# Kernel tuning notes

Hardware: AMD Instinct MI355X
Metric: run time of the kernel (lower is better)

The kernel has to match this reference:

```python
import jax, jax.numpy as jnp
import numpy as np

N_NODES = 40000
N_EDGES = 640000
BATCH = 2
IN_DIM = 3
HID = 128
OUT_DIM = 3


def setup_inputs() -> dict:
    key = jax.random.key(0)
    ks = jax.random.split(key, 16)
    p = jax.random.normal(ks[0], (BATCH, N_NODES, IN_DIM), dtype=jnp.float32)
    edge_rows = jax.random.randint(ks[1], (N_EDGES,), 0, N_NODES, dtype=jnp.int32)
    edge_cols = jax.random.randint(ks[2], (N_EDGES,), 0, N_NODES, dtype=jnp.int32)
    # normalize_sparse_matrix: divide each nonzero (value 1.0) by the row's nonzero count
    deg = jax.ops.segment_sum(jnp.ones((N_EDGES,), jnp.float32), edge_rows, num_segments=N_NODES)
    adj_vals = 1.0 / deg[edge_rows]  # every used row has deg >= 1
    s = 0.05
    # initial Linear(3 -> 128)
    W_init = jax.random.normal(ks[3], (IN_DIM, HID), jnp.float32) * s
    b_init = jnp.zeros((HID,), jnp.float32)
    # 4 GraphConvs inside the two blocks (all 128->128), each has filter + self_filter
    Wf_blocks = jax.random.normal(ks[4], (4, HID, HID), jnp.float32) * s
    bf_blocks = jnp.zeros((4, HID), jnp.float32)
    Ws_blocks = jax.random.normal(ks[5], (4, HID, HID), jnp.float32) * s
    bs_blocks = jnp.zeros((4, HID), jnp.float32)
    # final GraphConvLayer (128 -> 3)
    Wf_out = jax.random.normal(ks[6], (HID, OUT_DIM), jnp.float32) * s
    bf_out = jnp.zeros((OUT_DIM,), jnp.float32)
    Ws_out = jax.random.normal(ks[7], (HID, OUT_DIM), jnp.float32) * s
    bs_out = jnp.zeros((OUT_DIM,), jnp.float32)
    return dict(p=p, adj_vals=adj_vals, edge_rows=edge_rows, edge_cols=edge_cols,
                W_init=W_init, b_init=b_init,
                Wf_blocks=Wf_blocks, bf_blocks=bf_blocks,
                Ws_blocks=Ws_blocks, bs_blocks=bs_blocks,
                Wf_out=Wf_out, bf_out=bf_out, Ws_out=Ws_out, bs_out=bs_out)


def reference(p, adj_vals, edge_rows, edge_cols,
              W_init, b_init,
              Wf_blocks, bf_blocks, Ws_blocks, bs_blocks,
              Wf_out, bf_out, Ws_out, bs_out):
    n = p.shape[1]

    def spmm(xb):  # xb: [N, d] -> A @ xb via edge-list scatter-add
        return jax.ops.segment_sum(adj_vals[:, None] * xb[edge_cols], edge_rows, num_segments=n)

    spmm_b = jax.vmap(spmm)  # [B, N, d]

    def gconv(x, Wf, bf, Ws, bs):
        # sparse path: self_filter(x) + filter(spmm(adj, x))
        return (x @ Ws + bs) + (spmm_b(x) @ Wf + bf)

    x = p @ W_init + b_init  # [B, N, HID]
    for blk in range(2):  # two GraphConvBlocks, residual, no shortcut (dims equal)
        net = gconv(jax.nn.relu(x), Wf_blocks[2 * blk], bf_blocks[2 * blk],
                    Ws_blocks[2 * blk], bs_blocks[2 * blk])
        dx = gconv(jax.nn.relu(net), Wf_blocks[2 * blk + 1], bf_blocks[2 * blk + 1],
                   Ws_blocks[2 * blk + 1], bs_blocks[2 * blk + 1])
        x = x + dx
    # final GraphConvLayer 128 -> 3
    out = gconv(jax.nn.relu(x), Wf_out, bf_out, Ws_out, bs_out)
    return out
```

## Files before the change

### kernel.cpp

```cpp
#include <hip/hip_runtime.h>


typedef unsigned short u16;
typedef unsigned int   u32;
typedef __bf16 bf8_t __attribute__((ext_vector_type(8)));
typedef float  f4_t  __attribute__((ext_vector_type(4)));

#define N_NODES 40000
#define N_EDGES 640000
#define BN      80000

__device__ __forceinline__ float bf2f(u16 u) {
  union { u32 i; float f; } v; v.i = ((u32)u) << 16; return v.f;
}
__device__ __forceinline__ u16 f2bf(float f) {
  union { float f; u32 i; } v; v.f = f;
  u32 i = v.i;
  return (u16)((i + 0x7FFFu + ((i >> 16) & 1u)) >> 16);
}
__device__ __forceinline__ float asf(u32 i) {
  union { u32 u; float f; } v; v.u = i; return v.f;
}
__device__ __forceinline__ u32 pack2(float a, float b) {
  return (u32)f2bf(a) | ((u32)f2bf(b) << 16);
}

__global__ void fill_kernel(float* __restrict__ out, int n, float v) {
  int i = blockIdx.x * 256 + threadIdx.x;
  if (i < n) out[i] = v;
}

__global__ void hist_kernel(const int* __restrict__ rows, int* __restrict__ cnt) {
  int e = blockIdx.x * 256 + threadIdx.x;
  if (e < N_EDGES) atomicAdd(&cnt[rows[e]], 1);
}

__global__ void scan1_kernel(const int* __restrict__ cnt, int* __restrict__ row_ptr,
                             int* __restrict__ blocksum) {
  __shared__ int sm[256];
  int t = threadIdx.x;
  int row = blockIdx.x * 256 + t;
  int v = (row < N_NODES) ? cnt[row] : 0;
  sm[t] = v; __syncthreads();
  for (int off = 1; off < 256; off <<= 1) {
    int u = (t >= off) ? sm[t - off] : 0;
    __syncthreads();
    sm[t] += u;
    __syncthreads();
  }
  if (row < N_NODES) row_ptr[row] = sm[t] - v;
  if (t == 255) blocksum[blockIdx.x] = sm[255];
}

__global__ void scan2_kernel(int* __restrict__ blocksum, int* __restrict__ row_ptr, int nblk) {
  __shared__ int sm[256];
  int t = threadIdx.x;
  int v = (t < nblk) ? blocksum[t] : 0;
  sm[t] = v; __syncthreads();
  for (int off = 1; off < 256; off <<= 1) {
    int u = (t >= off) ? sm[t - off] : 0;
    __syncthreads();
    sm[t] += u;
    __syncthreads();
  }
  if (t < nblk) blocksum[t] = sm[t] - v;
  if (t == 255) row_ptr[N_NODES] = sm[255];
}

__global__ void scan3_kernel(int* __restrict__ row_ptr, const int* __restrict__ blocksum,
                             int* __restrict__ cnt) {
  int row = blockIdx.x * 256 + threadIdx.x;
  if (row < N_NODES) {
    int rp = row_ptr[row] + blocksum[blockIdx.x];
    row_ptr[row] = rp;
    cnt[row] = rp;
  }
}

__global__ void scatter_kernel(const int* __restrict__ rows, const int* __restrict__ cols,
                               int* __restrict__ cur, int* __restrict__ cols_s) {
  int e = blockIdx.x * 256 + threadIdx.x;
  if (e < N_EDGES) {
    int r = rows[e];
    int pos = atomicAdd(&cur[r], 1);
    cols_s[pos] = cols[e];
  }
}

__global__ void wprep_kernel(const float* __restrict__ Wf_b, const float* __restrict__ Ws_b,
                             const float* __restrict__ bf_b, const float* __restrict__ bs_b,
                             u16* __restrict__ WtCat, float* __restrict__ biasCat) {
  int idx = blockIdx.x * 256 + threadIdx.x;
  int g = idx >> 15, rem = idx & 32767;
  int h = rem >> 8, k = rem & 255;
  float v = (k < 128) ? Ws_b[(g * 128 + k) * 128 + h]
                      : Wf_b[(g * 128 + (k - 128)) * 128 + h];
  WtCat[idx] = f2bf(v);
  if (k == 0) biasCat[g * 128 + h] = bs_b[g * 128 + h] + bf_b[g * 128 + h];
}

__global__ void init_kernel(const float* __restrict__ p, const float* __restrict__ W,
                            const float* __restrict__ bias, u16* __restrict__ xb,
                            u16* __restrict__ rA) {
  int idx = blockIdx.x * 256 + threadIdx.x;
  int row = idx >> 6;
  int h = (idx & 63) * 2;
  float p0 = p[row * 3], p1 = p[row * 3 + 1], p2 = p[row * 3 + 2];
  float s0 = p0 * W[h]     + p1 * W[128 + h]     + p2 * W[256 + h]     + bias[h];
  float s1 = p0 * W[h + 1] + p1 * W[128 + h + 1] + p2 * W[256 + h + 1] + bias[h + 1];
  size_t o = (size_t)row * 64 + (h >> 1);
  ((u32*)xb)[o] = pack2(s0, s1);
  ((u32*)rA)[o] = pack2(s0 > 0.f ? s0 : 0.f, s1 > 0.f ? s1 : 0.f);
}

__global__ void spmm_kernel(const int* __restrict__ row_ptr, const int* __restrict__ cols_s,
                            const u16* __restrict__ xin, u16* __restrict__ yout) {
  int row = blockIdx.x * 4 + (threadIdx.x >> 6);
  int l = threadIdx.x & 63;
  int b = l >> 5, seg = l & 31;
  int s = row_ptr[row], e = row_ptr[row + 1];
  const u32* X = (const u32*)xin + (size_t)b * 2560000 + seg * 2;
  float a0 = 0.f, a1 = 0.f, a2 = 0.f, a3 = 0.f;
  int i = s;
  for (; i + 1 < e; i += 2) {
    int c0 = cols_s[i], c1 = cols_s[i + 1];
    uint2 u0 = *reinterpret_cast<const uint2*>(X + (size_t)c0 * 64);
    uint2 u1 = *reinterpret_cast<const uint2*>(X + (size_t)c1 * 64);
    a0 += asf(u0.x << 16); a1 += asf(u0.x & 0xffff0000u);
    a2 += asf(u0.y << 16); a3 += asf(u0.y & 0xffff0000u);
    a0 += asf(u1.x << 16); a1 += asf(u1.x & 0xffff0000u);
    a2 += asf(u1.y << 16); a3 += asf(u1.y & 0xffff0000u);
  }
  if (i < e) {
    int c = cols_s[i];
    uint2 u = *reinterpret_cast<const uint2*>(X + (size_t)c * 64);
    a0 += asf(u.x << 16); a1 += asf(u.x & 0xffff0000u);
    a2 += asf(u.y << 16); a3 += asf(u.y & 0xffff0000u);
  }
  float scale = (e > s) ? 1.f / (float)(e - s) : 0.f;
  uint2 o;
  o.x = pack2(a0 * scale, a1 * scale);
  o.y = pack2(a2 * scale, a3 * scale);
  *reinterpret_cast<uint2*>((u32*)yout + (size_t)b * 2560000 + (size_t)row * 64 + seg * 2) = o;
}

template <int MODE>
__global__ __launch_bounds__(256, 2) void gemm_kernel(
    const u16* __restrict__ rin, const u16* __restrict__ yin,
    const u16* __restrict__ WtCat, const float* __restrict__ biasCat, int g,
    u16* __restrict__ rout, u16* __restrict__ xresid) {
  __shared__ __align__(16) u16 ldsA[128 * 72];
  __shared__ __align__(16) u16 ldsW[128 * 72];
  int tid = threadIdx.x;
  int m0 = blockIdx.x * 128;
  int li = tid & 15, q = (tid >> 4) & 3, wv = tid >> 6;
  int wmo = (wv >> 1) * 64, wno = (wv & 1) * 64;

  f4_t acc[4][4];
#pragma unroll
  for (int i = 0; i < 4; ++i)
#pragma unroll
    for (int j = 0; j < 4; ++j) acc[i][j] = (f4_t){0.f, 0.f, 0.f, 0.f};

  const u16* Wsrc = WtCat + (size_t)g * 32768;

  for (int kb = 0; kb < 256; kb += 64) {
    __syncthreads();
    const u16* srcA = (kb < 128) ? (rin + kb) : (yin + (kb - 128));
#pragma unroll
    for (int p2 = 0; p2 < 4; ++p2) {
      int idx = p2 * 256 + tid;
      int row = idx >> 3, seg = idx & 7;
      uint4 va = *reinterpret_cast<const uint4*>(srcA + (size_t)(m0 + row) * 128 + seg * 8);
      *reinterpret_cast<uint4*>(&ldsA[row * 72 + seg * 8]) = va;
      uint4 vw = *reinterpret_cast<const uint4*>(Wsrc + (size_t)row * 256 + kb + seg * 8);
      *reinterpret_cast<uint4*>(&ldsW[row * 72 + seg * 8]) = vw;
    }
    __syncthreads();
#pragma unroll
    for (int kk = 0; kk < 64; kk += 32) {
      bf8_t af[4], wf[4];
#pragma unroll
      for (int t = 0; t < 4; ++t)
        af[t] = __builtin_bit_cast(bf8_t,
            *reinterpret_cast<const uint4*>(&ldsA[(wmo + t * 16 + li) * 72 + kk + q * 8]));
#pragma unroll
      for (int t = 0; t < 4; ++t)
        wf[t] = __builtin_bit_cast(bf8_t,
            *reinterpret_cast<const uint4*>(&ldsW[(wno + t * 16 + li) * 72 + kk + q * 8]));
#pragma unroll
      for (int i = 0; i < 4; ++i)
#pragma unroll
        for (int j = 0; j < 4; ++j)
          acc[i][j] = __builtin_amdgcn_mfma_f32_16x16x32_bf16(af[i], wf[j], acc[i][j], 0, 0, 0);
    }
  }

  float bias[4];
#pragma unroll
  for (int j = 0; j < 4; ++j) bias[j] = biasCat[g * 128 + wno + j * 16 + li];

#pragma unroll
  for (int i = 0; i < 4; ++i)
#pragma unroll
    for (int j = 0; j < 4; ++j)
#pragma unroll
      for (int r2 = 0; r2 < 4; ++r2) {
        int m = m0 + wmo + i * 16 + q * 4 + r2;
        int col = wno + j * 16 + li;
        float c = acc[i][j][r2] + bias[j];
        size_t id = (size_t)m * 128 + col;
        if (MODE == 0) {
          rout[id] = f2bf(c > 0.f ? c : 0.f);
        } else {
          float xn = bf2f(xresid[id]) + c;
          xresid[id] = f2bf(xn);
          rout[id] = f2bf(xn > 0.f ? xn : 0.f);
        }
      }
}

__global__ void final_kernel(const u16* __restrict__ rA, const u16* __restrict__ y,
                             const float* __restrict__ Wso, const float* __restrict__ Wfo,
                             const float* __restrict__ bso, const float* __restrict__ bfo,
                             float* __restrict__ out) {
  int row = blockIdx.x * 4 + (threadIdx.x >> 6);
  int l = threadIdx.x & 63;
  u32 ra = ((const u32*)rA)[(size_t)row * 64 + l];
  u32 yv = ((const u32*)y)[(size_t)row * 64 + l];
  float r0 = asf(ra << 16), r1 = asf(ra & 0xffff0000u);
  float y0 = asf(yv << 16), y1 = asf(yv & 0xffff0000u);
  int ch = l * 2;
  float p0 = r0 * Wso[ch * 3 + 0] + y0 * Wfo[ch * 3 + 0] + r1 * Wso[ch * 3 + 3] + y1 * Wfo[ch * 3 + 3];
  float p1 = r0 * Wso[ch * 3 + 1] + y0 * Wfo[ch * 3 + 1] + r1 * Wso[ch * 3 + 4] + y1 * Wfo[ch * 3 + 4];
  float p2 = r0 * Wso[ch * 3 + 2] + y0 * Wfo[ch * 3 + 2] + r1 * Wso[ch * 3 + 5] + y1 * Wfo[ch * 3 + 5];
#pragma unroll
  for (int off = 32; off >= 1; off >>= 1) {
    p0 += __shfl_down(p0, off);
    p1 += __shfl_down(p1, off);
    p2 += __shfl_down(p2, off);
  }
  if (l == 0) {
    out[row * 3 + 0] = p0 + bso[0] + bfo[0];
    out[row * 3 + 1] = p1 + bso[1] + bfo[1];
    out[row * 3 + 2] = p2 + bso[2] + bfo[2];
  }
}

extern "C" void kernel_launch(void* const* d_in, const int* in_sizes, int n_in,
                              void* d_out, int out_size, void* d_ws, size_t ws_size,
                              hipStream_t stream) {
  float* out = (float*)d_out;
  int fill_grid = (out_size + 255) / 256;

  const int exp_sizes[14] = {240000, 640000, 640000, 640000, 384, 128,
                             65536, 512, 65536, 512, 384, 3, 384, 3};
  bool sizes_ok = (n_in == 14);
  if (sizes_ok) for (int i = 0; i < 14; ++i) if (in_sizes[i] != exp_sizes[i]) sizes_ok = false;
  if (!sizes_ok) {
    fill_kernel<<<fill_grid, 256, 0, stream>>>(out, out_size, 1.0f);
    return;
  }

  const size_t NEED = (size_t)4 * BN * 128 * 2 + (size_t)N_EDGES * 4 + 160016 + 160000 + 1024 + 262144 + 2048;
  if (ws_size < NEED) {
    fill_kernel<<<fill_grid, 256, 0, stream>>>(out, out_size, 0.0f);
    return;
  }

  const float* p      = (const float*)d_in[0];
  const int*   erows  = (const int*)d_in[2];
  const int*   ecols  = (const int*)d_in[3];
  const float* W_init = (const float*)d_in[4];
  const float* b_init = (const float*)d_in[5];
  const float* Wf_b   = (const float*)d_in[6];
  const float* bf_b   = (const float*)d_in[7];
  const float* Ws_b   = (const float*)d_in[8];
  const float* bs_b   = (const float*)d_in[9];
  const float* Wf_o   = (const float*)d_in[10];
  const float* bf_o   = (const float*)d_in[11];
  const float* Ws_o   = (const float*)d_in[12];
  const float* bs_o   = (const float*)d_in[13];

  char* w = (char*)d_ws;
  u16*   rA       = (u16*)w;   w += (size_t)BN * 128 * 2;
  u16*   rB       = (u16*)w;   w += (size_t)BN * 128 * 2;
  u16*   y        = (u16*)w;   w += (size_t)BN * 128 * 2;
  u16*   xb       = (u16*)w;   w += (size_t)BN * 128 * 2;
  int*   cols_s   = (int*)w;   w += (size_t)N_EDGES * 4;
  int*   row_ptr  = (int*)w;   w += 160016;
  int*   cnt      = (int*)w;   w += 160000;
  int*   blocksum = (int*)w;   w += 1024;
  u16*   WtCat    = (u16*)w;   w += 4 * 128 * 256 * 2;
  float* biasCat  = (float*)w; w += 4 * 128 * 4;

  const int NBLK = (N_NODES + 255) / 256;

  hipMemsetAsync(cnt, 0, N_NODES * 4, stream);
  hist_kernel<<<2500, 256, 0, stream>>>(erows, cnt);
  scan1_kernel<<<NBLK, 256, 0, stream>>>(cnt, row_ptr, blocksum);
  scan2_kernel<<<1, 256, 0, stream>>>(blocksum, row_ptr, NBLK);
  scan3_kernel<<<NBLK, 256, 0, stream>>>(row_ptr, blocksum, cnt);
  scatter_kernel<<<2500, 256, 0, stream>>>(erows, ecols, cnt, cols_s);
  wprep_kernel<<<512, 256, 0, stream>>>(Wf_b, Ws_b, bf_b, bs_b, WtCat, biasCat);
  init_kernel<<<20000, 256, 0, stream>>>(p, W_init, b_init, xb, rA);

  for (int blk = 0; blk < 2; ++blk) {
    spmm_kernel<<<10000, 256, 0, stream>>>(row_ptr, cols_s, rA, y);
    gemm_kernel<0><<<625, 256, 0, stream>>>(rA, y, WtCat, biasCat, 2 * blk, rB, nullptr);
    spmm_kernel<<<10000, 256, 0, stream>>>(row_ptr, cols_s, rB, y);
    gemm_kernel<1><<<625, 256, 0, stream>>>(rB, y, WtCat, biasCat, 2 * blk + 1, rA, xb);
  }
  spmm_kernel<<<10000, 256, 0, stream>>>(row_ptr, cols_s, rA, y);
  final_kernel<<<20000, 256, 0, stream>>>(rA, y, Ws_o, Wf_o, bs_o, bf_o, out);
}
```

Before: 510.0 us.

## Reassociate final layer to project before SpMM, widen SpMM loads, prefetch GEMM tiles

The final GraphConv now projects the 128-wide activations down to 3 channels first and only then aggregates over neighbours, using A(xW) = (Ax)W. This replaces a full 128-wide SpMM with a 3-wide one. The block SpMM now splits the batch across thread blocks and has each lane load 16-byte rows, with four lane groups handling different edges and combining through cross-lane shuffles. The GEMM adds register prefetch of the next K tile so global loads overlap the MFMA work. The reassociation changes rounding slightly, since the projection is taken from bf16 activations before aggregation.

```diff
diff --git a/kernel.cpp b/kernel.cpp
--- a/kernel.cpp
+++ b/kernel.cpp
@@ -113,35 +113,51 @@
   ((u32*)rA)[o] = pack2(s0 > 0.f ? s0 : 0.f, s1 > 0.f ? s1 : 0.f);
 }
 
+#define ACC8(u)                                                           \
+  a0 += asf((u).x << 16); a1 += asf((u).x & 0xffff0000u);                 \
+  a2 += asf((u).y << 16); a3 += asf((u).y & 0xffff0000u);                 \
+  a4 += asf((u).z << 16); a5 += asf((u).z & 0xffff0000u);                 \
+  a6 += asf((u).w << 16); a7 += asf((u).w & 0xffff0000u);
+
 __global__ void spmm_kernel(const int* __restrict__ row_ptr, const int* __restrict__ cols_s,
                             const u16* __restrict__ xin, u16* __restrict__ yout) {
-  int row = blockIdx.x * 4 + (threadIdx.x >> 6);
+  int b = blockIdx.x & 1;
+  int row = (blockIdx.x >> 1) * 4 + (threadIdx.x >> 6);
   int l = threadIdx.x & 63;
-  int b = l >> 5, seg = l & 31;
+  int g = l >> 4, sl = l & 15;
   int s = row_ptr[row], e = row_ptr[row + 1];
-  const u32* X = (const u32*)xin + (size_t)b * 2560000 + seg * 2;
-  float a0 = 0.f, a1 = 0.f, a2 = 0.f, a3 = 0.f;
+  const uint4* X = (const uint4*)xin + (size_t)b * 640000 + sl;
+  float a0 = 0.f, a1 = 0.f, a2 = 0.f, a3 = 0.f, a4 = 0.f, a5 = 0.f, a6 = 0.f, a7 = 0.f;
   int i = s;
-  for (; i + 1 < e; i += 2) {
-    int c0 = cols_s[i], c1 = cols_s[i + 1];
-    uint2 u0 = *reinterpret_cast<const uint2*>(X + (size_t)c0 * 64);
-    uint2 u1 = *reinterpret_cast<const uint2*>(X + (size_t)c1 * 64);
-    a0 += asf(u0.x << 16); a1 += asf(u0.x & 0xffff0000u);
-    a2 += asf(u0.y << 16); a3 += asf(u0.y & 0xffff0000u);
-    a0 += asf(u1.x << 16); a1 += asf(u1.x & 0xffff0000u);
-    a2 += asf(u1.y << 16); a3 += asf(u1.y & 0xffff0000u);
-  }
-  if (i < e) {
-    int c = cols_s[i];
-    uint2 u = *reinterpret_cast<const uint2*>(X + (size_t)c * 64);
-    a0 += asf(u.x << 16); a1 += asf(u.x & 0xffff0000u);
-    a2 += asf(u.y << 16); a3 += asf(u.y & 0xffff0000u);
-  }
-  float scale = (e > s) ? 1.f / (float)(e - s) : 0.f;
-  uint2 o;
-  o.x = pack2(a0 * scale, a1 * scale);
-  o.y = pack2(a2 * scale, a3 * scale);
-  *reinterpret_cast<uint2*>((u32*)yout + (size_t)b * 2560000 + (size_t)row * 64 + seg * 2) = o;
+  for (; i + 7 < e; i += 8) {
+    int c0 = cols_s[i + g], c1 = cols_s[i + 4 + g];
+    uint4 u0 = X[(size_t)c0 * 16];
+    uint4 u1 = X[(size_t)c1 * 16];
+    ACC8(u0); ACC8(u1);
+  }
+  for (; i + 3 < e; i += 4) {
+    int c = cols_s[i + g];
+    uint4 u = X[(size_t)c * 16];
+    ACC8(u);
+  }
+  if (i + g < e) {
+    int c = cols_s[i + g];
+    uint4 u = X[(size_t)c * 16];
+    ACC8(u);
+  }
+  a0 += __shfl_xor(a0, 16); a1 += __shfl_xor(a1, 16); a2 += __shfl_xor(a2, 16); a3 += __shfl_xor(a3, 16);
+  a4 += __shfl_xor(a4, 16); a5 += __shfl_xor(a5, 16); a6 += __shfl_xor(a6, 16); a7 += __shfl_xor(a7, 16);
+  a0 += __shfl_xor(a0, 32); a1 += __shfl_xor(a1, 32); a2 += __shfl_xor(a2, 32); a3 += __shfl_xor(a3, 32);
+  a4 += __shfl_xor(a4, 32); a5 += __shfl_xor(a5, 32); a6 += __shfl_xor(a6, 32); a7 += __shfl_xor(a7, 32);
+  if (g == 0) {
+    float sc = (e > s) ? 1.f / (float)(e - s) : 0.f;
+    uint4 o;
+    o.x = pack2(a0 * sc, a1 * sc);
+    o.y = pack2(a2 * sc, a3 * sc);
+    o.z = pack2(a4 * sc, a5 * sc);
+    o.w = pack2(a6 * sc, a7 * sc);
+    *((uint4*)yout + (size_t)b * 640000 + (size_t)row * 16 + sl) = o;
+  }
 }
 
 template <int MODE>
@@ -164,19 +180,33 @@
 
   const u16* Wsrc = WtCat + (size_t)g * 32768;
 
+  uint4 pa[4], pw[4];
+#pragma unroll
+  for (int p2 = 0; p2 < 4; ++p2) {
+    int idx = p2 * 256 + tid, row = idx >> 3, seg = idx & 7;
+    pa[p2] = *reinterpret_cast<const uint4*>(rin + (size_t)(m0 + row) * 128 + seg * 8);
+    pw[p2] = *reinterpret_cast<const uint4*>(Wsrc + (size_t)row * 256 + seg * 8);
+  }
+
   for (int kb = 0; kb < 256; kb += 64) {
     __syncthreads();
-    const u16* srcA = (kb < 128) ? (rin + kb) : (yin + (kb - 128));
 #pragma unroll
     for (int p2 = 0; p2 < 4; ++p2) {
-      int idx = p2 * 256 + tid;
-      int row = idx >> 3, seg = idx & 7;
-      uint4 va = *reinterpret_cast<const uint4*>(srcA + (size_t)(m0 + row) * 128 + seg * 8);
-      *reinterpret_cast<uint4*>(&ldsA[row * 72 + seg * 8]) = va;
-      uint4 vw = *reinterpret_cast<const uint4*>(Wsrc + (size_t)row * 256 + kb + seg * 8);
-      *reinterpret_cast<uint4*>(&ldsW[row * 72 + seg * 8]) = vw;
+      int idx = p2 * 256 + tid, row = idx >> 3, seg = idx & 7;
+      *reinterpret_cast<uint4*>(&ldsA[row * 72 + seg * 8]) = pa[p2];
+      *reinterpret_cast<uint4*>(&ldsW[row * 72 + seg * 8]) = pw[p2];
     }
     __syncthreads();
+    if (kb < 192) {
+      int kn = kb + 64;
+      const u16* srcA = (kn < 128) ? (rin + kn) : (yin + (kn - 128));
+#pragma unroll
+      for (int p2 = 0; p2 < 4; ++p2) {
+        int idx = p2 * 256 + tid, row = idx >> 3, seg = idx & 7;
+        pa[p2] = *reinterpret_cast<const uint4*>(srcA + (size_t)(m0 + row) * 128 + seg * 8);
+        pw[p2] = *reinterpret_cast<const uint4*>(Wsrc + (size_t)row * 256 + kn + seg * 8);
+      }
+    }
 #pragma unroll
     for (int kk = 0; kk < 64; kk += 32) {
       bf8_t af[4], wf[4];
@@ -220,31 +250,51 @@
       }
 }
 
-__global__ void final_kernel(const u16* __restrict__ rA, const u16* __restrict__ y,
-                             const float* __restrict__ Wso, const float* __restrict__ Wfo,
-                             const float* __restrict__ bso, const float* __restrict__ bfo,
-                             float* __restrict__ out) {
+__global__ void zproj_kernel(const u16* __restrict__ rA,
+                             const float* __restrict__ Wfo, const float* __restrict__ Wso,
+                             const float* __restrict__ bfo, const float* __restrict__ bso,
+                             float4* __restrict__ zf4, float4* __restrict__ zs4) {
   int row = blockIdx.x * 4 + (threadIdx.x >> 6);
   int l = threadIdx.x & 63;
   u32 ra = ((const u32*)rA)[(size_t)row * 64 + l];
-  u32 yv = ((const u32*)y)[(size_t)row * 64 + l];
   float r0 = asf(ra << 16), r1 = asf(ra & 0xffff0000u);
-  float y0 = asf(yv << 16), y1 = asf(yv & 0xffff0000u);
   int ch = l * 2;
-  float p0 = r0 * Wso[ch * 3 + 0] + y0 * Wfo[ch * 3 + 0] + r1 * Wso[ch * 3 + 3] + y1 * Wfo[ch * 3 + 3];
-  float p1 = r0 * Wso[ch * 3 + 1] + y0 * Wfo[ch * 3 + 1] + r1 * Wso[ch * 3 + 4] + y1 * Wfo[ch * 3 + 4];
-  float p2 = r0 * Wso[ch * 3 + 2] + y0 * Wfo[ch * 3 + 2] + r1 * Wso[ch * 3 + 5] + y1 * Wfo[ch * 3 + 5];
+  float f0 = r0 * Wfo[ch * 3 + 0] + r1 * Wfo[ch * 3 + 3];
+  float f1 = r0 * Wfo[ch * 3 + 1] + r1 * Wfo[ch * 3 + 4];
+  float f2 = r0 * Wfo[ch * 3 + 2] + r1 * Wfo[ch * 3 + 5];
+  float s0 = r0 * Wso[ch * 3 + 0] + r1 * Wso[ch * 3 + 3];
+  float s1 = r0 * Wso[ch * 3 + 1] + r1 * Wso[ch * 3 + 4];
+  float s2 = r0 * Wso[ch * 3 + 2] + r1 * Wso[ch * 3 + 5];
 #pragma unroll
   for (int off = 32; off >= 1; off >>= 1) {
-    p0 += __shfl_down(p0, off);
-    p1 += __shfl_down(p1, off);
-    p2 += __shfl_down(p2, off);
+    f0 += __shfl_down(f0, off); f1 += __shfl_down(f1, off); f2 += __shfl_down(f2, off);
+    s0 += __shfl_down(s0, off); s1 += __shfl_down(s1, off); s2 += __shfl_down(s2, off);
   }
   if (l == 0) {
-    out[row * 3 + 0] = p0 + bso[0] + bfo[0];
-    out[row * 3 + 1] = p1 + bso[1] + bfo[1];
-    out[row * 3 + 2] = p2 + bso[2] + bfo[2];
-  }
+    zf4[row] = make_float4(f0, f1, f2, 0.f);
+    zs4[row] = make_float4(s0 + bso[0] + bfo[0], s1 + bso[1] + bfo[1], s2 + bso[2] + bfo[2], 0.f);
+  }
+}
+
+__global__ void spmm3_kernel(const int* __restrict__ row_ptr, const int* __restrict__ cols_s,
+                             const float4* __restrict__ zf4, const float4* __restrict__ zs4,
+                             float* __restrict__ out) {
+  int idx = blockIdx.x * 256 + threadIdx.x;
+  if (idx >= BN) return;
+  int b = (idx >= N_NODES) ? 1 : 0;
+  int r = idx - b * N_NODES;
+  int s = row_ptr[r], e = row_ptr[r + 1];
+  const float4* Z = zf4 + (size_t)b * N_NODES;
+  float a0 = 0.f, a1 = 0.f, a2 = 0.f;
+  for (int i = s; i < e; ++i) {
+    float4 z = Z[cols_s[i]];
+    a0 += z.x; a1 += z.y; a2 += z.z;
+  }
+  float sc = (e > s) ? 1.f / (float)(e - s) : 0.f;
+  float4 zs = zs4[idx];
+  out[idx * 3 + 0] = zs.x + a0 * sc;
+  out[idx * 3 + 1] = zs.y + a1 * sc;
+  out[idx * 3 + 2] = zs.z + a2 * sc;
 }
 
 extern "C" void kernel_launch(void* const* d_in, const int* in_sizes, int n_in,
@@ -294,6 +344,9 @@
   u16*   WtCat    = (u16*)w;   w += 4 * 128 * 256 * 2;
   float* biasCat  = (float*)w; w += 4 * 128 * 4;
 
+  float4* zf4 = (float4*)y;
+  float4* zs4 = (float4*)(y + 640000);
+
   const int NBLK = (N_NODES + 255) / 256;
 
   hipMemsetAsync(cnt, 0, N_NODES * 4, stream);
@@ -306,11 +359,11 @@
   init_kernel<<<20000, 256, 0, stream>>>(p, W_init, b_init, xb, rA);
 
   for (int blk = 0; blk < 2; ++blk) {
-    spmm_kernel<<<10000, 256, 0, stream>>>(row_ptr, cols_s, rA, y);
+    spmm_kernel<<<20000, 256, 0, stream>>>(row_ptr, cols_s, rA, y);
     gemm_kernel<0><<<625, 256, 0, stream>>>(rA, y, WtCat, biasCat, 2 * blk, rB, nullptr);
-    spmm_kernel<<<10000, 256, 0, stream>>>(row_ptr, cols_s, rB, y);
+    spmm_kernel<<<20000, 256, 0, stream>>>(row_ptr, cols_s, rB, y);
     gemm_kernel<1><<<625, 256, 0, stream>>>(rB, y, WtCat, biasCat, 2 * blk + 1, rA, xb);
   }
-  spmm_kernel<<<10000, 256, 0, stream>>>(row_ptr, cols_s, rA, y);
-  final_kernel<<<20000, 256, 0, stream>>>(rA, y, Ws_o, Wf_o, bs_o, bf_o, out);
-}
+  zproj_kernel<<<20000, 256, 0, stream>>>(rA, Wf_o, Ws_o, bf_o, bs_o, zf4, zs4);
+  spmm3_kernel<<<(BN + 255) / 256, 256, 0, stream>>>(row_ptr, cols_s, zf4, zs4, out);
+}
```

Result: slower. 538.5 us (+5.6%).
